# Kernel optimization log

Measured on AMD Instinct MI355X. Metric: run time of the kernel, lower is better.

## Reference

```python
import jax, jax.numpy as jnp
import numpy as np

V, E, H = 50257, 512, 1024  # vocab, embed_dim, hidden_dim
B, S = 64, 2048             # batch, src_len


def setup_inputs() -> dict:
    key = jax.random.key(0)
    ks = jax.random.split(key, 16)
    sc = 0.02
    emb = jax.random.normal(ks[0], (V, E), jnp.float32) * sc
    emb = emb.at[0].set(0.0)  # padding_idx=0
    return {
        "x": jax.random.randint(ks[1], (B, 1), 0, V),
        "hidden": jax.random.normal(ks[2], (1, B, H), jnp.float32),
        "cell": jax.random.normal(ks[3], (1, B, H), jnp.float32),
        "encoder_outputs": jax.random.normal(ks[4], (B, S, H), jnp.float32),
        "emb": emb,
        "Wa_w": jax.random.normal(ks[5], (H, H), jnp.float32) * sc,
        "Wa_b": jnp.zeros((H,), jnp.float32),
        "Ua_w": jax.random.normal(ks[6], (H, H), jnp.float32) * sc,
        "Ua_b": jnp.zeros((H,), jnp.float32),
        "va_w": jax.random.normal(ks[7], (1, H), jnp.float32) * sc,
        "va_b": jnp.zeros((1,), jnp.float32),
        "Wih": jax.random.normal(ks[8], (4 * H, E + H), jnp.float32) * sc,
        "Whh": jax.random.normal(ks[9], (4 * H, H), jnp.float32) * sc,
        "bih": jnp.zeros((4 * H,), jnp.float32),
        "bhh": jnp.zeros((4 * H,), jnp.float32),
        "fc_w": jax.random.normal(ks[10], (V, H), jnp.float32) * sc,
        "fc_b": jnp.zeros((V,), jnp.float32),
    }


def reference(x, hidden, cell, encoder_outputs, emb, Wa_w, Wa_b, Ua_w, Ua_b,
              va_w, va_b, Wih, Whh, bih, bhh, fc_w, fc_b):
    # Embedding lookup: [B,1] -> [B,E]
    embedded = emb[x[:, 0]]
    # Bahdanau additive attention
    s_t = hidden[-1]                                          # [B,H]
    proj_s = jnp.einsum('bh,oh->bo', s_t, Wa_w) + Wa_b        # [B,H]
    proj_e = jnp.einsum('bsh,oh->bso', encoder_outputs, Ua_w) + Ua_b  # [B,S,H]
    e = jnp.tanh(proj_s[:, None, :] + proj_e)                 # [B,S,H]
    scores = jnp.einsum('bsh,h->bs', e, va_w[0]) + va_b[0]    # [B,S]
    attn = jax.nn.softmax(scores, axis=1)                     # [B,S]
    context = jnp.einsum('bs,bsh->bh', attn, encoder_outputs)  # [B,H]
    # Single-step LSTM (torch gate order: i, f, g, o)
    lstm_in = jnp.concatenate([embedded, context], axis=1)    # [B,E+H]
    gates = lstm_in @ Wih.T + bih + s_t @ Whh.T + bhh         # [B,4H]
    i, f, g, o = jnp.split(gates, 4, axis=1)
    i, f, o = jax.nn.sigmoid(i), jax.nn.sigmoid(f), jax.nn.sigmoid(o)
    g = jnp.tanh(g)
    c_new = f * cell[-1] + i * g
    h_new = o * jnp.tanh(c_new)
    predictions = (h_new @ fc_w.T + fc_b)[:, None, :]          # [B,1,V]
    return predictions, h_new[None], c_new[None]
```

## Files before the change

kernel.cpp:

```cpp
#include <hip/hip_runtime.h>
#include <hip/hip_bf16.h>

#define V_ 50257
#define H_ 1024
#define S_ 2048

typedef float f32x4 __attribute__((ext_vector_type(4)));
typedef short s16x8 __attribute__((ext_vector_type(8)));

__device__ __forceinline__ unsigned short f2bf(float f){
  unsigned u = __builtin_bit_cast(unsigned, f);
  return (unsigned short)((u + 0x7FFFu + ((u >> 16) & 1u)) >> 16);
}
__device__ __forceinline__ unsigned cvt2(float a, float b){
  return (unsigned)f2bf(a) | ((unsigned)f2bf(b) << 16);
}
__device__ __forceinline__ float bf2f(unsigned short h){
  return __builtin_bit_cast(float, (unsigned)h << 16);
}
__device__ __forceinline__ float fast_tanh(float x){
  return 1.0f - 2.0f/(__expf(2.0f*x)+1.0f);
}
__device__ __forceinline__ float fast_sig(float x){
  return 1.0f/(1.0f+__expf(-x));
}
__device__ __forceinline__ void gld_lds16(const void* g, void* l){
  __builtin_amdgcn_global_load_lds((const __attribute__((address_space(1))) void*)g,
                                   (__attribute__((address_space(3))) void*)l, 16, 0, 0);
}

#define BAR() do { __builtin_amdgcn_sched_barrier(0); __builtin_amdgcn_s_barrier(); __builtin_amdgcn_sched_barrier(0); } while(0)
#define VMW4() asm volatile("s_waitcnt vmcnt(4)" ::: "memory")
#define VMW0() asm volatile("s_waitcnt vmcnt(0)" ::: "memory")

__global__ __launch_bounds__(256) void k_cvt_bf16(const float* __restrict__ src,
                                                  unsigned short* __restrict__ dst, int n){
  int i = (blockIdx.x*256 + threadIdx.x)*4;
  if (i < n){
    float4 f = *(const float4*)(src + i);
    uint2 u;
    u.x = cvt2(f.x, f.y);
    u.y = cvt2(f.z, f.w);
    *(uint2*)(dst + i) = u;
  }
}

__global__ __launch_bounds__(256) void k_cvt_enc(const float* __restrict__ src,
                                                 unsigned short* __restrict__ dst){
  const size_t stride = (size_t)gridDim.x * 256;
  const float4* s4 = (const float4*)src;
  uint2* d2 = (uint2*)dst;
  for (size_t i = (size_t)blockIdx.x*256 + threadIdx.x; i < 33554432u; i += stride){
    float4 f = s4[i];
    uint2 u;
    u.x = cvt2(f.x, f.y);
    u.y = cvt2(f.z, f.w);
    d2[i] = u;
  }
}

__global__ __launch_bounds__(1024,4) void k_proje256(
    const unsigned short* __restrict__ A,
    const unsigned short* __restrict__ Bw,
    const float* __restrict__ ps,
    const float* __restrict__ Ua_b,
    const float* __restrict__ va,
    float* __restrict__ part)
{
  extern __shared__ unsigned short smem[];
  const int t = threadIdx.x;
  const int lane = t & 63, wid = t >> 6;
  const int lr = lane & 15, lk = lane >> 4;
  const int wr = wid >> 2, wc = wid & 3;

  int bid = blockIdx.x;
  int L = (bid & 7) * 256 + (bid >> 3);
  const int wgm = L >> 2, wgn = L & 3;
  const int m0 = wgm * 256, n0 = wgn * 256;

  const int srow = lane >> 3;
  const int schunk = (lane & 7) ^ srow;

  f32x4 acc[4][4] = {};
  s16x8 af[4], bfr[4];

  auto STAGE = [&](int slot, int kt){
    #pragma unroll
    for (int h = 0; h < 4; ++h){
      const unsigned short* gsrc = (h < 2) ? A : Bw;
      const size_t g0 = (h < 2) ? (size_t)m0 : (size_t)n0;
      unsigned short* ldst = smem + ((h < 2) ? 0 : 32768) + slot*16384;
      int rb = (h & 1)*128 + wid*8;
      gld_lds16(gsrc + (g0 + rb + srow)*1024 + kt*64 + schunk*8,
                ldst + rb*64);
    }
  };

#define SUBPH(As_, Bs_, ks) do { \
    _Pragma("unroll") \
    for (int ni = 0; ni < 4; ++ni){ \
      int rl = wc*64 + ni*16 + lr; \
      bfr[ni] = *(const s16x8*)((Bs_) + rl*64 + ((((ks)*4+lk) ^ (lr&7))*8)); \
    } \
    _Pragma("unroll") \
    for (int mi = 0; mi < 4; ++mi){ \
      int rl = wr*64 + mi*16 + lr; \
      af[mi] = *(const s16x8*)((As_) + rl*64 + ((((ks)*4+lk) ^ (lr&7))*8)); \
    } \
    __builtin_amdgcn_s_setprio(1); \
    _Pragma("unroll") \
    for (int mi = 0; mi < 4; ++mi) \
      _Pragma("unroll") \
      for (int ni = 0; ni < 4; ++ni) \
        acc[mi][ni] = __builtin_amdgcn_mfma_f32_16x16x32_bf16(af[mi], bfr[ni], acc[mi][ni], 0,0,0); \
    __builtin_amdgcn_s_setprio(0); \
  } while(0)

#define HALF(slot) do { \
    const unsigned short* As_ = smem + (slot)*16384; \
    const unsigned short* Bs_ = smem + 32768 + (slot)*16384; \
    SUBPH(As_, Bs_, 0); \
    SUBPH(As_, Bs_, 1); \
  } while(0)

  STAGE(0, 0);
  STAGE(1, 1);
  VMW4(); BAR();

  for (int i = 0; i < 8; ++i){
    HALF(0);
    if (i < 7){
      BAR();
      STAGE(0, 2*i + 2);
      VMW4();
      BAR();
    } else {
      VMW0();
      BAR();
    }
    HALF(1);
    if (i < 7){
      BAR();
      STAGE(1, 2*i + 3);
      VMW4();
      BAR();
    }
  }

  const int b = m0 >> 11;
  float psv[4], vav[4];
  #pragma unroll
  for (int ni = 0; ni < 4; ++ni){
    int n = n0 + wc*64 + ni*16 + lr;
    psv[ni] = ps[b*1024 + n] + Ua_b[n];
    vav[ni] = va[n];
  }
  #pragma unroll
  for (int mi = 0; mi < 4; ++mi){
    float p0=0.f,p1=0.f,p2=0.f,p3=0.f;
    #pragma unroll
    for (int ni = 0; ni < 4; ++ni){
      p0 += vav[ni]*fast_tanh(acc[mi][ni][0] + psv[ni]);
      p1 += vav[ni]*fast_tanh(acc[mi][ni][1] + psv[ni]);
      p2 += vav[ni]*fast_tanh(acc[mi][ni][2] + psv[ni]);
      p3 += vav[ni]*fast_tanh(acc[mi][ni][3] + psv[ni]);
    }
    #pragma unroll
    for (int off = 1; off < 16; off <<= 1){
      p0 += __shfl_xor(p0, off);
      p1 += __shfl_xor(p1, off);
      p2 += __shfl_xor(p2, off);
      p3 += __shfl_xor(p3, off);
    }
    if (lr == 0){
      int rg = m0 + wr*64 + mi*16 + lk*4;
      int slot = wgn*4 + wc;
      part[(size_t)rg*16 + slot]     = p0;
      part[(size_t)(rg+1)*16 + slot] = p1;
      part[(size_t)(rg+2)*16 + slot] = p2;
      part[(size_t)(rg+3)*16 + slot] = p3;
    }
  }
#undef SUBPH
#undef HALF
}

__global__ __launch_bounds__(256,2) void k_proje_f32(
    const float* __restrict__ A,
    const unsigned short* __restrict__ Bw,
    const float* __restrict__ ps,
    const float* __restrict__ Ua_b,
    const float* __restrict__ va,
    float* __restrict__ part)
{
  __shared__ unsigned char sm[32768];
  const int t = threadIdx.x;
  const int lane = t & 63, wid = t >> 6;
  const int lr = lane & 15, lk = lane >> 4;
  int bid = blockIdx.x;
  int L = (bid & 7) * 1024 + (bid >> 3);
  const int wgm = L >> 3, wgn = L & 7;
  const int m0 = wgm * 128, n0 = wgn * 128;
  const int wm = wid >> 1, wn = wid & 1;

  f32x4 acc[4][4] = {};
  const int row2 = t >> 1, half = t & 1;
  const float* aSrc = A + (size_t)(m0 + row2) * 1024 + half * 32;
  const unsigned short* bSrc = Bw + (size_t)(n0 + row2) * 1024 + half * 32;
  unsigned char* Al = sm;
  unsigned char* Bl = sm + 16384;
  const int swzr = row2 & 7;

  for (int kt = 0; kt < 16; ++kt){
    __syncthreads();
    #pragma unroll
    for (int c = 0; c < 4; ++c){
      float4 f0 = *(const float4*)(aSrc + kt*64 + c*8);
      float4 f1 = *(const float4*)(aSrc + kt*64 + c*8 + 4);
      union { unsigned u[4]; s16x8 v; } p;
      p.u[0]=cvt2(f0.x,f0.y); p.u[1]=cvt2(f0.z,f0.w);
      p.u[2]=cvt2(f1.x,f1.y); p.u[3]=cvt2(f1.z,f1.w);
      int ch = half*4 + c;
      *(s16x8*)(Al + row2*128 + ((ch ^ swzr)*16)) = p.v;
    }
    #pragma unroll
    for (int c = 0; c < 4; ++c){
      s16x8 v = *(const s16x8*)(bSrc + kt*64 + (half*4 + c)*8);
      *(s16x8*)(Bl + row2*128 + (((half*4+c) ^ swzr)*16)) = v;
    }
    __syncthreads();
    #pragma unroll
    for (int ks = 0; ks < 2; ++ks){
      s16x8 af[4], bfr[4];
      #pragma unroll
      for (int mi = 0; mi < 4; ++mi){
        int r = wm*64 + mi*16 + lr;
        af[mi] = *(const s16x8*)(Al + r*128 + (((ks*4+lk) ^ (lr&7))*16));
      }
      #pragma unroll
      for (int ni = 0; ni < 4; ++ni){
        int r = wn*64 + ni*16 + lr;
        bfr[ni] = *(const s16x8*)(Bl + r*128 + (((ks*4+lk) ^ (lr&7))*16));
      }
      #pragma unroll
      for (int mi = 0; mi < 4; ++mi)
        #pragma unroll
        for (int ni = 0; ni < 4; ++ni)
          acc[mi][ni] = __builtin_amdgcn_mfma_f32_16x16x32_bf16(af[mi], bfr[ni], acc[mi][ni], 0,0,0);
    }
  }
  const int b = m0 >> 11;
  float psv[4], vav[4];
  #pragma unroll
  for (int ni = 0; ni < 4; ++ni){
    int n = n0 + wn*64 + ni*16 + lr;
    psv[ni] = ps[b*1024 + n] + Ua_b[n];
    vav[ni] = va[n];
  }
  #pragma unroll
  for (int mi = 0; mi < 4; ++mi){
    float p0=0.f,p1=0.f,p2=0.f,p3=0.f;
    #pragma unroll
    for (int ni = 0; ni < 4; ++ni){
      p0 += vav[ni]*fast_tanh(acc[mi][ni][0] + psv[ni]);
      p1 += vav[ni]*fast_tanh(acc[mi][ni][1] + psv[ni]);
      p2 += vav[ni]*fast_tanh(acc[mi][ni][2] + psv[ni]);
      p3 += vav[ni]*fast_tanh(acc[mi][ni][3] + psv[ni]);
    }
    #pragma unroll
    for (int off = 1; off < 16; off <<= 1){
      p0 += __shfl_xor(p0, off);
      p1 += __shfl_xor(p1, off);
      p2 += __shfl_xor(p2, off);
      p3 += __shfl_xor(p3, off);
    }
    if (lr == 0){
      int rg = m0 + wm*64 + mi*16 + lk*4;
      int slot = wgn*2 + wn;
      part[(size_t)rg*16 + slot]     = p0;
      part[(size_t)(rg+1)*16 + slot] = p1;
      part[(size_t)(rg+2)*16 + slot] = p2;
      part[(size_t)(rg+3)*16 + slot] = p3;
    }
  }
}

__global__ __launch_bounds__(256,2) void k_gemm64(
    const float* __restrict__ A,
    const float* __restrict__ B1,
    const float* __restrict__ B2,
    const float* __restrict__ bias1,
    const float* __restrict__ bias2,
    float* __restrict__ C, int ldC,
    int N, int K, int K1)
{
  __shared__ unsigned char sm[16384];
  const int t = threadIdx.x;
  const int lane = t & 63, wid = t >> 6;
  const int lr = lane & 15, lk = lane >> 4;
  const int n0 = blockIdx.x * 64;
  f32x4 acc[4] = {};
  const int row = t >> 2, seg = t & 3;
  unsigned char* Al = sm;
  unsigned char* Bl = sm + 8192;
  const int swzr = row & 7;
  const int K2 = K - K1;

  for (int k0 = 0; k0 < K; k0 += 64){
    __syncthreads();
    {
      const float* s = A + (size_t)row*K + k0 + seg*16;
      #pragma unroll
      for (int c = 0; c < 2; ++c){
        float4 f0 = *(const float4*)(s + c*8);
        float4 f1 = *(const float4*)(s + c*8 + 4);
        union { unsigned u[4]; s16x8 v; } p;
        p.u[0]=cvt2(f0.x,f0.y); p.u[1]=cvt2(f0.z,f0.w);
        p.u[2]=cvt2(f1.x,f1.y); p.u[3]=cvt2(f1.z,f1.w);
        *(s16x8*)(Al + row*128 + (((seg*2+c) ^ swzr)*16)) = p.v;
      }
    }
    {
      int n = n0 + row;
      #pragma unroll
      for (int c = 0; c < 2; ++c){
        union { unsigned u[4]; s16x8 v; } p;
        if (n < N){
          int k = k0 + seg*16 + c*8;
          const float* s;
          if (k < K1) s = B1 + (size_t)n*K1 + k;
          else        s = B2 + (size_t)n*K2 + (k - K1);
          float4 f0 = *(const float4*)(s);
          float4 f1 = *(const float4*)(s + 4);
          p.u[0]=cvt2(f0.x,f0.y); p.u[1]=cvt2(f0.z,f0.w);
          p.u[2]=cvt2(f1.x,f1.y); p.u[3]=cvt2(f1.z,f1.w);
        } else {
          p.u[0]=0u; p.u[1]=0u; p.u[2]=0u; p.u[3]=0u;
        }
        *(s16x8*)(Bl + row*128 + (((seg*2+c) ^ swzr)*16)) = p.v;
      }
    }
    __syncthreads();
    #pragma unroll
    for (int ks = 0; ks < 2; ++ks){
      s16x8 bfr = *(const s16x8*)(Bl + (wid*16+lr)*128 + (((ks*4+lk) ^ (lr&7))*16));
      #pragma unroll
      for (int mi = 0; mi < 4; ++mi){
        s16x8 af = *(const s16x8*)(Al + (mi*16+lr)*128 + (((ks*4+lk) ^ (lr&7))*16));
        acc[mi] = __builtin_amdgcn_mfma_f32_16x16x32_bf16(af, bfr, acc[mi], 0,0,0);
      }
    }
  }
  int n = n0 + wid*16 + lr;
  if (n < N){
    float bv = (bias1 ? bias1[n] : 0.f) + (bias2 ? bias2[n] : 0.f);
    #pragma unroll
    for (int mi = 0; mi < 4; ++mi){
      #pragma unroll
      for (int r = 0; r < 4; ++r){
        C[(size_t)(mi*16 + lk*4 + r)*ldC + n] = acc[mi][r] + bv;
      }
    }
  }
}

__global__ __launch_bounds__(256) void k_softmax(const float* __restrict__ part,
                                                 const float* __restrict__ va_b,
                                                 float* __restrict__ attn){
  __shared__ float sc[2048];
  __shared__ float red[8];
  const int b = blockIdx.x, t = threadIdx.x;
  float vb = va_b[0];
  float lmax = -1e30f;
  #pragma unroll
  for (int j = 0; j < 8; ++j){
    int s = t + j*256;
    const float* p = part + ((size_t)b*2048 + s)*16;
    float v = vb;
    #pragma unroll
    for (int i = 0; i < 16; ++i) v += p[i];
    sc[s] = v;
    lmax = fmaxf(lmax, v);
  }
  for (int off = 32; off; off >>= 1) lmax = fmaxf(lmax, __shfl_xor(lmax, off));
  if ((t&63)==0) red[t>>6] = lmax;
  __syncthreads();
  float m = fmaxf(fmaxf(red[0],red[1]),fmaxf(red[2],red[3]));
  float lsum = 0.f;
  #pragma unroll
  for (int j = 0; j < 8; ++j){
    int s = t + j*256;
    float e = __expf(sc[s]-m);
    sc[s] = e; lsum += e;
  }
  for (int off = 32; off; off >>= 1) lsum += __shfl_xor(lsum, off);
  if ((t&63)==0) red[4 + (t>>6)] = lsum;
  __syncthreads();
  float inv = 1.f/(red[4]+red[5]+red[6]+red[7]);
  #pragma unroll
  for (int j = 0; j < 8; ++j){
    int s = t + j*256;
    attn[(size_t)b*2048+s] = sc[s]*inv;
  }
}

__global__ __launch_bounds__(256) void k_context_bf(const float* __restrict__ attn,
                                                    const unsigned short* __restrict__ encb,
                                                    float* __restrict__ ctxp){
  const int b = blockIdx.x >> 4, scid = blockIdx.x & 15;
  const int t = threadIdx.x;
  float a0=0.f,a1=0.f,a2=0.f,a3=0.f;
  const unsigned short* e = encb + ((size_t)b*2048 + scid*128)*1024 + t*4;
  const float* at = attn + (size_t)b*2048 + scid*128;
  #pragma unroll 4
  for (int s = 0; s < 128; ++s){
    float a = at[s];
    ushort4 v = *(const ushort4*)(e + (size_t)s*1024);
    a0 += a*bf2f(v.x); a1 += a*bf2f(v.y); a2 += a*bf2f(v.z); a3 += a*bf2f(v.w);
  }
  float4 o; o.x=a0; o.y=a1; o.z=a2; o.w=a3;
  *(float4*)(ctxp + ((size_t)scid*64 + b)*1024 + t*4) = o;
}

__global__ __launch_bounds__(256) void k_context_f32(const float* __restrict__ attn,
                                                     const float* __restrict__ enc,
                                                     float* __restrict__ ctxp){
  const int b = blockIdx.x >> 4, scid = blockIdx.x & 15;
  const int t = threadIdx.x;
  float a0=0.f,a1=0.f,a2=0.f,a3=0.f;
  const float* e = enc + ((size_t)b*2048 + scid*128)*1024;
  const float* at = attn + (size_t)b*2048 + scid*128;
  for (int s = 0; s < 128; ++s){
    float a = at[s];
    const float* er = e + (size_t)s*1024;
    a0 += a*er[t]; a1 += a*er[t+256]; a2 += a*er[t+512]; a3 += a*er[t+768];
  }
  float* o = ctxp + ((size_t)scid*64 + b)*1024;
  o[t]=a0; o[t+256]=a1; o[t+512]=a2; o[t+768]=a3;
}

__global__ __launch_bounds__(256) void k_build(const int* __restrict__ x,
                                               const float* __restrict__ emb,
                                               const float* __restrict__ ctxp,
                                               const float* __restrict__ hidden,
                                               float* __restrict__ lstm){
  const int b = blockIdx.x, t = threadIdx.x;
  int xe = x[b];
  for (int col = t; col < 2560; col += 256){
    float v;
    if (col < 512) v = emb[(size_t)xe*512 + col];
    else if (col < 1536){
      int h = col - 512;
      v = 0.f;
      #pragma unroll
      for (int i = 0; i < 16; ++i) v += ctxp[((size_t)i*64 + b)*1024 + h];
    } else v = hidden[(size_t)b*1024 + (col-1536)];
    lstm[(size_t)b*2560 + col] = v;
  }
}

__global__ __launch_bounds__(256) void k_lstm(const float* __restrict__ gates,
                                              const float* __restrict__ cell,
                                              float* __restrict__ out){
  int idx = blockIdx.x*256 + threadIdx.x;
  int b = idx >> 10, h = idx & 1023;
  const float* g = gates + (size_t)b*4096;
  float gi = fast_sig(g[h]);
  float gf = fast_sig(g[h+1024]);
  float gg = fast_tanh(g[h+2048]);
  float go = fast_sig(g[h+3072]);
  float c  = gf*cell[idx] + gi*gg;
  float hn = go*fast_tanh(c);
  out[(size_t)V_*64 + idx]         = hn;
  out[(size_t)V_*64 + 65536 + idx] = c;
}

extern "C" void kernel_launch(void* const* d_in, const int* in_sizes, int n_in,
                              void* d_out, int out_size, void* d_ws, size_t ws_size,
                              hipStream_t stream){
  const int*   x     = (const int*)d_in[0];
  const float* hidden= (const float*)d_in[1];
  const float* cell  = (const float*)d_in[2];
  const float* enc   = (const float*)d_in[3];
  const float* emb   = (const float*)d_in[4];
  const float* Wa_w  = (const float*)d_in[5];
  const float* Wa_b  = (const float*)d_in[6];
  const float* Ua_w  = (const float*)d_in[7];
  const float* Ua_b  = (const float*)d_in[8];
  const float* va_w  = (const float*)d_in[9];
  const float* va_b  = (const float*)d_in[10];
  const float* Wih   = (const float*)d_in[11];
  const float* Whh   = (const float*)d_in[12];
  const float* bih   = (const float*)d_in[13];
  const float* bhh   = (const float*)d_in[14];
  const float* fc_w  = (const float*)d_in[15];
  const float* fc_b  = (const float*)d_in[16];
  float* out = (float*)d_out;
  char* ws = (char*)d_ws;
  unsigned short* ua_bf = (unsigned short*)(ws + 0);
  float* ps    = (float*)(ws + 2097152);
  float* attn  = (float*)(ws + 2359296);
  float* lstm  = (float*)(ws + 2883584);
  float* gates = (float*)(ws + 3538944);
  float* part  = (float*)(ws + 6684672);
  float* ctxp  = (float*)(ws + 10878976);
  unsigned short* enc_bf = (unsigned short*)(ws + 16777216);
  const size_t REQ = 16777216u + 268435456u;

  hipLaunchKernelGGL(k_cvt_bf16, dim3(1024), dim3(256), 0, stream, Ua_w, ua_bf, 1048576);
  hipLaunchKernelGGL(k_gemm64, dim3(16), dim3(256), 0, stream,
                     hidden, Wa_w, nullptr, Wa_b, nullptr, ps, 1024, 1024, 1024, 1024);
  if (ws_size >= REQ){
    hipLaunchKernelGGL(k_cvt_enc, dim3(8192), dim3(256), 0, stream, enc, enc_bf);
    hipLaunchKernelGGL(k_proje256, dim3(2048), dim3(1024), 131072, stream,
                       enc_bf, ua_bf, ps, Ua_b, va_w, part);
    hipLaunchKernelGGL(k_softmax, dim3(64), dim3(256), 0, stream, part, va_b, attn);
    hipLaunchKernelGGL(k_context_bf, dim3(1024), dim3(256), 0, stream, attn, enc_bf, ctxp);
  } else {
    hipLaunchKernelGGL(k_proje_f32, dim3(8192), dim3(256), 0, stream,
                       enc, ua_bf, ps, Ua_b, va_w, part);
    hipLaunchKernelGGL(k_softmax, dim3(64), dim3(256), 0, stream, part, va_b, attn);
    hipLaunchKernelGGL(k_context_f32, dim3(1024), dim3(256), 0, stream, attn, enc, ctxp);
  }
  hipLaunchKernelGGL(k_build, dim3(64), dim3(256), 0, stream, x, emb, ctxp, hidden, lstm);
  hipLaunchKernelGGL(k_gemm64, dim3(64), dim3(256), 0, stream,
                     lstm, Wih, Whh, bih, bhh, gates, 4096, 4096, 2560, 1536);
  hipLaunchKernelGGL(k_lstm, dim3(256), dim3(256), 0, stream, gates, cell, out);
  hipLaunchKernelGGL(k_gemm64, dim3(786), dim3(256), 0, stream,
                     out + (size_t)V_*64, fc_w, nullptr, fc_b, nullptr, out, V_, V_, 1024, 1024);
}
```

Measured before the change: 678.9 us.

## Replace FC GEMM with direct-from-global bf16 MFMA kernel using pre-converted hidden

The LSTM kernel now also writes a bf16 copy of h_new into workspace. A new FC kernel has each wave own 64 vocab rows, stream fc_w straight from global memory, convert it to bf16 in registers, and run MFMA against the bf16 hidden rows, skipping the LDS staging of the generic GEMM. The aim is to make the 200MB fc_w read bandwidth-bound with less sync overhead. In exchange it relies on uncoalesced row-strided loads and repeated A-fragment global reads, and output stores are strided by V.

```diff
diff --git a/kernel.cpp b/kernel.cpp
--- a/kernel.cpp
+++ b/kernel.cpp
@@ -364,6 +364,58 @@
   }
 }
 
+__global__ __launch_bounds__(256) void k_fc(
+    const unsigned short* __restrict__ hbf,
+    const float* __restrict__ fcw,
+    const float* __restrict__ fcb,
+    float* __restrict__ out)
+{
+  const int t = threadIdx.x;
+  const int lane = t & 63, wid = t >> 6;
+  const int lr = lane & 15, lk = lane >> 4;
+  const int v0 = blockIdx.x*256 + wid*64;
+  f32x4 acc[4][4] = {};
+  const int vl[4] = { v0 + 0*16 + lr, v0 + 1*16 + lr, v0 + 2*16 + lr, v0 + 3*16 + lr };
+
+  for (int kt = 0; kt < 32; ++kt){
+    s16x8 afr[4];
+    #pragma unroll
+    for (int mi = 0; mi < 4; ++mi)
+      afr[mi] = *(const s16x8*)(hbf + (size_t)(mi*16 + lr)*1024 + kt*32 + lk*8);
+    #pragma unroll
+    for (int vt = 0; vt < 4; ++vt){
+      union { unsigned u[4]; s16x8 v; } p;
+      if (vl[vt] < V_){
+        const float* s = fcw + (size_t)vl[vt]*1024 + kt*32 + lk*8;
+        float4 f0 = *(const float4*)(s);
+        float4 f1 = *(const float4*)(s + 4);
+        p.u[0]=cvt2(f0.x,f0.y); p.u[1]=cvt2(f0.z,f0.w);
+        p.u[2]=cvt2(f1.x,f1.y); p.u[3]=cvt2(f1.z,f1.w);
+      } else {
+        p.u[0]=0u; p.u[1]=0u; p.u[2]=0u; p.u[3]=0u;
+      }
+      #pragma unroll
+      for (int mi = 0; mi < 4; ++mi)
+        acc[vt][mi] = __builtin_amdgcn_mfma_f32_16x16x32_bf16(afr[mi], p.v, acc[vt][mi], 0,0,0);
+    }
+  }
+  #pragma unroll
+  for (int vt = 0; vt < 4; ++vt){
+    int v = vl[vt];
+    if (v < V_){
+      float bv = fcb[v];
+      #pragma unroll
+      for (int mi = 0; mi < 4; ++mi){
+        #pragma unroll
+        for (int r = 0; r < 4; ++r){
+          int b = mi*16 + lk*4 + r;
+          out[(size_t)b*V_ + v] = acc[vt][mi][r] + bv;
+        }
+      }
+    }
+  }
+}
+
 __global__ __launch_bounds__(256) void k_softmax(const float* __restrict__ part,
                                                  const float* __restrict__ va_b,
                                                  float* __restrict__ attn){
@@ -461,7 +513,8 @@
 
 __global__ __launch_bounds__(256) void k_lstm(const float* __restrict__ gates,
                                               const float* __restrict__ cell,
-                                              float* __restrict__ out){
+                                              float* __restrict__ out,
+                                              unsigned short* __restrict__ hbf){
   int idx = blockIdx.x*256 + threadIdx.x;
   int b = idx >> 10, h = idx & 1023;
   const float* g = gates + (size_t)b*4096;
@@ -473,6 +526,7 @@
   float hn = go*fast_tanh(c);
   out[(size_t)V_*64 + idx]         = hn;
   out[(size_t)V_*64 + 65536 + idx] = c;
+  hbf[idx] = f2bf(hn);
 }
 
 extern "C" void kernel_launch(void* const* d_in, const int* in_sizes, int n_in,
@@ -504,6 +558,7 @@
   float* gates = (float*)(ws + 3538944);
   float* part  = (float*)(ws + 6684672);
   float* ctxp  = (float*)(ws + 10878976);
+  unsigned short* h_bf = (unsigned short*)(ws + 15073280);
   unsigned short* enc_bf = (unsigned short*)(ws + 16777216);
   const size_t REQ = 16777216u + 268435456u;
 
@@ -525,7 +580,6 @@
   hipLaunchKernelGGL(k_build, dim3(64), dim3(256), 0, stream, x, emb, ctxp, hidden, lstm);
   hipLaunchKernelGGL(k_gemm64, dim3(64), dim3(256), 0, stream,
                      lstm, Wih, Whh, bih, bhh, gates, 4096, 4096, 2560, 1536);
-  hipLaunchKernelGGL(k_lstm, dim3(256), dim3(256), 0, stream, gates, cell, out);
-  hipLaunchKernelGGL(k_gemm64, dim3(786), dim3(256), 0, stream,
-                     out + (size_t)V_*64, fc_w, nullptr, fc_b, nullptr, out, V_, V_, 1024, 1024);
-}
+  hipLaunchKernelGGL(k_lstm, dim3(256), dim3(256), 0, stream, gates, cell, out, h_bf);
+  hipLaunchKernelGGL(k_fc, dim3(786), dim3(256), 0, stream, h_bf, fc_w, fc_b, out);
+}
```

After: 727.5 us. 7.2% more time.
